# Kernel optimization log

Hardware: AMD Instinct MI355X
Metric: run time of the kernel (lower is better)

The kernel has to match this reference:

```python
import jax, jax.numpy as jnp
import numpy as np

B, N, IN_DIM, HID, OUT, E = 2, 50000, 64, 256, 128, 500000

def setup_inputs() -> dict:
    key = jax.random.key(0)
    ks = jax.random.split(key, 8)
    s = lambda fan_in: 1.0 / np.sqrt(fan_in)
    x = jax.random.normal(ks[0], (B, N, IN_DIM), dtype=jnp.float32)
    edges = jax.random.randint(ks[1], (E, 2), 0, N, dtype=jnp.int64)
    return {
        "x": x,
        "edges": edges,
        "ew1": jax.random.normal(ks[2], (2 * IN_DIM, HID), dtype=jnp.float32) * s(2 * IN_DIM),
        "eb1": jnp.zeros((HID,), jnp.float32),
        "ew2": jax.random.normal(ks[3], (HID, OUT), dtype=jnp.float32) * s(HID),
        "eb2": jnp.zeros((OUT,), jnp.float32),
        "nw1": jax.random.normal(ks[4], (IN_DIM, HID), dtype=jnp.float32) * s(IN_DIM),
        "nb1": jnp.zeros((HID,), jnp.float32),
        "nw2": jax.random.normal(ks[5], (HID, OUT), dtype=jnp.float32) * s(HID),
        "nb2": jnp.zeros((OUT,), jnp.float32),
        "dw": jax.random.normal(ks[6], (OUT, IN_DIM), dtype=jnp.float32) * s(OUT),
        "db": jnp.zeros((IN_DIM,), jnp.float32),
    }

def _mlp(z, w1, b1, w2, b2):
    return jax.nn.relu(z @ w1 + b1) @ w2 + b2

def reference(x, edges, ew1, eb1, ew2, eb2, nw1, nb1, nw2, nb2, dw, db):
    u, v = edges[:, 0], edges[:, 1]
    # node embedding: [B, N, OUT]
    h = _mlp(x, nw1, nb1, nw2, nb2)
    # per-edge MLP on concatenated endpoint features: [B, E, OUT]
    edge_input = jnp.concatenate([x[:, u], x[:, v]], axis=-1)  # [B, E, 2*IN]
    edge_emb = _mlp(edge_input, ew1, eb1, ew2, eb2)
    # scatter-add edge message to both endpoints
    messages = jnp.zeros_like(h).at[:, u].add(edge_emb).at[:, v].add(edge_emb)
    h = h + messages
    recon = h @ dw + db  # [B, N, IN]
    return recon
```

## Files before the change

### kernel.cpp

```cpp
#include <hip/hip_runtime.h>
#include <hip/hip_bf16.h>

#define BB   2
#define NN   50000
#define BN   100000
#define NE   500000
#define NSB  196

using u16 = unsigned short;
using u32 = unsigned int;
typedef __attribute__((ext_vector_type(8))) short short8;
typedef __attribute__((ext_vector_type(4))) float f32x4;

__device__ __forceinline__ u16 f2bf(float f) {
    union { float f; u32 u; } w; w.f = f;
    return (u16)((w.u + 0x7fffu + ((w.u >> 16) & 1u)) >> 16);
}

#if defined(__has_builtin)
#if __has_builtin(__builtin_amdgcn_cvt_pk_bf16_f32)
#define HAVE_CVTPK 1
#endif
#endif

__device__ __forceinline__ u32 pack_bf(float lo, float hi) {
#ifdef HAVE_CVTPK
    auto r = __builtin_amdgcn_cvt_pk_bf16_f32(lo, hi);
    u32 out; __builtin_memcpy(&out, &r, sizeof(out));
    return out;
#else
    return ((u32)f2bf(hi) << 16) | (u32)f2bf(lo);
#endif
}

__global__ __launch_bounds__(256) void csr_zero(int* __restrict__ cursor) {
    int i = blockIdx.x * 256 + threadIdx.x;
    if (i < NN) cursor[i] = 0;
}

__global__ __launch_bounds__(256) void csr_hist(const int* __restrict__ edges,
                                                int* __restrict__ cursor) {
    int e = blockIdx.x * 256 + threadIdx.x;
    if (e < NE) {
        atomicAdd(&cursor[edges[2*e]], 1);
        atomicAdd(&cursor[edges[2*e+1]], 1);
    }
}

__global__ __launch_bounds__(256) void scan_pass1(const int* __restrict__ cursor,
                                                  int* __restrict__ bsum) {
    __shared__ int s[256];
    const int t = threadIdx.x;
    int i = blockIdx.x * 256 + t;
    s[t] = (i < NN) ? cursor[i] : 0;
    __syncthreads();
    for (int d = 128; d > 0; d >>= 1) {
        if (t < d) s[t] += s[t + d];
        __syncthreads();
    }
    if (t == 0) bsum[blockIdx.x] = s[0];
}

__global__ __launch_bounds__(256) void scan_pass2(const int* __restrict__ bsum,
                                                  int* __restrict__ boff) {
    __shared__ int s[256];
    const int t = threadIdx.x;
    s[t] = (t < NSB) ? bsum[t] : 0;
    __syncthreads();
    for (int d = 1; d < 256; d <<= 1) {
        int v = (t >= d) ? s[t - d] : 0;
        __syncthreads();
        s[t] += v;
        __syncthreads();
    }
    if (t <= NSB) boff[t] = (t == 0) ? 0 : s[t - 1];
}

__global__ __launch_bounds__(256) void scan_pass3(int* __restrict__ cursor,
                                                  const int* __restrict__ boff,
                                                  int* __restrict__ off) {
    __shared__ int s[256];
    const int t = threadIdx.x;
    int i = blockIdx.x * 256 + t;
    int v = (i < NN) ? cursor[i] : 0;
    s[t] = v;
    __syncthreads();
    for (int d = 1; d < 256; d <<= 1) {
        int p = (t >= d) ? s[t - d] : 0;
        __syncthreads();
        s[t] += p;
        __syncthreads();
    }
    int excl = boff[blockIdx.x] + s[t] - v;
    if (i < NN) { off[i] = excl; cursor[i] = excl; }
    if (i == NN - 1) off[NN] = excl + v;
}

__global__ __launch_bounds__(256) void csr_fill(const int* __restrict__ edges,
                                                int* __restrict__ cursor,
                                                int* __restrict__ pos) {
    int e = blockIdx.x * 256 + threadIdx.x;
    if (e < NE) {
        pos[2*e]     = atomicAdd(&cursor[edges[2*e]], 1);
        pos[2*e + 1] = atomicAdd(&cursor[edges[2*e+1]], 1);
    }
}

__global__ __launch_bounds__(256) void weight_prep(
    const float* __restrict__ ew1, const float* __restrict__ nw1,
    const float* __restrict__ ew2, const float* __restrict__ nw2,
    const float* __restrict__ dw,  const float* __restrict__ db,
    const float* __restrict__ eb2, const float* __restrict__ nb2,
    u16* __restrict__ frag, float* __restrict__ bias2)
{
    int blk = blockIdx.x, t = threadIdx.x;
    if (blk < 192) {
        int idx = blk * 256 + t;
        const float* src; int KB, local;
        if (idx < 32768) { local = idx;         src = ew1; KB = 4; }
        else             { local = idx - 32768; src = nw1; KB = 2; }
        int j = local & 7, l = (local >> 3) & 63, rest = local >> 9;
        int kblk = rest % KB, ntile = rest / KB;
        int n = ntile * 16 + (l & 15);
        int k = kblk * 32 + ((l >> 4) << 3) + j;
        frag[idx] = f2bf(src[k * 256 + n]);
    } else if (blk < 320) {
        int idx = (blk - 192) * 256 + t;
        const float* src = (idx < 16384) ? ew2 : nw2;
        int local = idx & 16383;
        int j = local & 7, l = (local >> 3) & 63, rest = local >> 9;
        int kblk = rest & 7, ntile = rest >> 3;
        int n = ntile * 16 + (l & 15);
        int k = kblk * 32 + ((l >> 4) << 3) + j;
        float s = 0.f;
        for (int jj = 0; jj < 128; ++jj) s = fmaf(src[k * 128 + jj], dw[jj * 64 + n], s);
        frag[49152 + idx] = f2bf(s);
    } else if (t < 128) {
        int d = t & 63;
        const float* bsrc = (t >= 64) ? nb2 : eb2;
        float s = 0.f;
        #pragma unroll 4
        for (int j = 0; j < 128; ++j) s = fmaf(bsrc[j], dw[j * 64 + d], s);
        if (t >= 64) bias2[64 + d] = s + db[d];
        else         bias2[d] = s;
    }
}

__global__ __launch_bounds__(256) void node_mlp_kernel(
    const float* __restrict__ x, const float* __restrict__ nb1,
    const float* __restrict__ bias2, const u16* __restrict__ frag,
    u16* __restrict__ xbf, float* __restrict__ out)
{
    __shared__ u16 xs[64 * 64];
    __shared__ u16 hid[64 * 256];
    const int t = threadIdx.x;
    const int wave = t >> 6, l = t & 63, lane15 = l & 15, quad = l >> 4;
    const int r0 = blockIdx.x * 64;
    const int valid = min(64, BN - r0);

    #pragma unroll
    for (int it = 0; it < 4; ++it) {
        int i = t + it * 256;
        int m = i >> 4, c4 = i & 15;
        int row = min(r0 + m, BN - 1);
        float4 g = ((const float4*)x)[(size_t)row * 16 + c4];
        uint2 q = make_uint2(pack_bf(g.x, g.y), pack_bf(g.z, g.w));
        int chunk = c4 >> 1;
        *(uint2*)(xs + m * 64 + ((chunk ^ (m & 7)) << 3) + (c4 & 1) * 4) = q;
        *(uint2*)(xbf + (size_t)row * 64 + c4 * 4) = q;
    }
    __syncthreads();

    {
        f32x4 acc[4][4];
        #pragma unroll
        for (int i = 0; i < 4; ++i)
            #pragma unroll
            for (int mt = 0; mt < 4; ++mt) acc[i][mt] = f32x4{0.f,0.f,0.f,0.f};
        const u16* w1 = frag + 32768;
        #pragma unroll
        for (int kblk = 0; kblk < 2; ++kblk) {
            short8 bf[4], af[4];
            int chunk = kblk * 4 + quad;
            #pragma unroll
            for (int mt = 0; mt < 4; ++mt) {
                int row = mt*16 + lane15;
                bf[mt] = *(const short8*)(xs + row * 64 + ((chunk ^ (row & 7)) << 3));
            }
            #pragma unroll
            for (int i = 0; i < 4; ++i)
                af[i] = *(const short8*)(w1 + (((wave*4 + i)*2 + kblk)*64 + l) * 8);
            #pragma unroll
            for (int i = 0; i < 4; ++i)
                #pragma unroll
                for (int mt = 0; mt < 4; ++mt)
                    acc[i][mt] = __builtin_amdgcn_mfma_f32_16x16x32_bf16(af[i], bf[mt], acc[i][mt], 0, 0, 0);
        }
        #pragma unroll
        for (int i = 0; i < 4; ++i) {
            int n0 = (wave*4 + i)*16 + quad*4;
            int chunk = (wave*4 + i)*2 + (quad >> 1);
            float4 bv = *(const float4*)(nb1 + n0);
            #pragma unroll
            for (int mt = 0; mt < 4; ++mt) {
                int row = mt*16 + lane15;
                uint2 q = make_uint2(
                    pack_bf(fmaxf(acc[i][mt][0] + bv.x, 0.f), fmaxf(acc[i][mt][1] + bv.y, 0.f)),
                    pack_bf(fmaxf(acc[i][mt][2] + bv.z, 0.f), fmaxf(acc[i][mt][3] + bv.w, 0.f)));
                *(uint2*)(hid + row * 256 + ((chunk ^ (row & 15)) << 3) + (quad & 1) * 4) = q;
            }
        }
    }
    __syncthreads();

    {
        f32x4 acc[4];
        #pragma unroll
        for (int mt = 0; mt < 4; ++mt) acc[mt] = f32x4{0.f,0.f,0.f,0.f};
        const u16* w2 = frag + 65536;
        #pragma unroll
        for (int kblk = 0; kblk < 8; ++kblk) {
            short8 bf[4], af;
            int chunk = kblk * 4 + quad;
            #pragma unroll
            for (int mt = 0; mt < 4; ++mt) {
                int row = mt*16 + lane15;
                bf[mt] = *(const short8*)(hid + row * 256 + ((chunk ^ (row & 15)) << 3));
            }
            af = *(const short8*)(w2 + ((wave*8 + kblk)*64 + l) * 8);
            #pragma unroll
            for (int mt = 0; mt < 4; ++mt)
                acc[mt] = __builtin_amdgcn_mfma_f32_16x16x32_bf16(af, bf[mt], acc[mt], 0, 0, 0);
        }
        int n0 = wave*16 + quad*4;
        float4 bv = *(const float4*)(bias2 + 64 + n0);
        #pragma unroll
        for (int mt = 0; mt < 4; ++mt) {
            int m = mt*16 + lane15;
            if (m < valid) {
                float4 o;
                o.x = acc[mt][0] + bv.x; o.y = acc[mt][1] + bv.y;
                o.z = acc[mt][2] + bv.z; o.w = acc[mt][3] + bv.w;
                *(float4*)(out + (size_t)(r0 + m) * 64 + n0) = o;
            }
        }
    }
}

__global__ __launch_bounds__(256) void edge_emb_kernel(
    const u16* __restrict__ xbf, const int* __restrict__ edges,
    const float* __restrict__ eb1, const float* __restrict__ bias2,
    const u16* __restrict__ frag, const int* __restrict__ pos,
    u16* __restrict__ perm, int b_base, size_t pstride16)
{
    __shared__ u16 ein[64 * 128];
    __shared__ u16 hid[64 * 256];
    __shared__ int us[64], vs[64], ps[64], qs[64];
    const int t = threadIdx.x;
    const int wave = t >> 6, l = t & 63, lane15 = l & 15, quad = l >> 4;
    const int b = b_base + blockIdx.y;
    u16* permb = perm + pstride16 * blockIdx.y;
    const int e0 = blockIdx.x * 64;
    const int valid = min(64, NE - e0);

    if (t < 64) {
        int e = min(e0 + t, NE - 1);
        us[t] = edges[2 * e];
        vs[t] = edges[2 * e + 1];
        ps[t] = pos[2 * e];
        qs[t] = pos[2 * e + 1];
    }
    __syncthreads();

    #pragma unroll
    for (int it = 0; it < 4; ++it) {
        int i = t + it * 256;
        int m = i >> 4, c = i & 15;
        int half = c >> 3, c8 = c & 7;
        int node = half ? vs[m] : us[m];
        uint4 q = ((const uint4*)xbf)[(size_t)(b * NN + node) * 8 + c8];
        *(uint4*)(ein + m * 128 + ((c ^ (m & 15)) << 3)) = q;
    }
    __syncthreads();

    {
        f32x4 acc[4][4];
        #pragma unroll
        for (int i = 0; i < 4; ++i)
            #pragma unroll
            for (int mt = 0; mt < 4; ++mt) acc[i][mt] = f32x4{0.f,0.f,0.f,0.f};
        const u16* w1 = frag;
        #pragma unroll
        for (int kblk = 0; kblk < 4; ++kblk) {
            short8 bf[4], af[4];
            int chunk = kblk * 4 + quad;
            #pragma unroll
            for (int mt = 0; mt < 4; ++mt) {
                int row = mt*16 + lane15;
                bf[mt] = *(const short8*)(ein + row * 128 + ((chunk ^ (row & 15)) << 3));
            }
            #pragma unroll
            for (int i = 0; i < 4; ++i)
                af[i] = *(const short8*)(w1 + (((wave*4 + i)*4 + kblk)*64 + l) * 8);
            #pragma unroll
            for (int i = 0; i < 4; ++i)
                #pragma unroll
                for (int mt = 0; mt < 4; ++mt)
                    acc[i][mt] = __builtin_amdgcn_mfma_f32_16x16x32_bf16(af[i], bf[mt], acc[i][mt], 0, 0, 0);
        }
        #pragma unroll
        for (int i = 0; i < 4; ++i) {
            int n0 = (wave*4 + i)*16 + quad*4;
            int chunk = (wave*4 + i)*2 + (quad >> 1);
            float4 bv = *(const float4*)(eb1 + n0);
            #pragma unroll
            for (int mt = 0; mt < 4; ++mt) {
                int row = mt*16 + lane15;
                uint2 q = make_uint2(
                    pack_bf(fmaxf(acc[i][mt][0] + bv.x, 0.f), fmaxf(acc[i][mt][1] + bv.y, 0.f)),
                    pack_bf(fmaxf(acc[i][mt][2] + bv.z, 0.f), fmaxf(acc[i][mt][3] + bv.w, 0.f)));
                *(uint2*)(hid + row * 256 + ((chunk ^ (row & 15)) << 3) + (quad & 1) * 4) = q;
            }
        }
    }
    __syncthreads();

    {
        f32x4 acc[4];
        #pragma unroll
        for (int mt = 0; mt < 4; ++mt) acc[mt] = f32x4{0.f,0.f,0.f,0.f};
        const u16* w2 = frag + 49152;
        #pragma unroll
        for (int kblk = 0; kblk < 8; ++kblk) {
            short8 bf[4], af;
            int chunk = kblk * 4 + quad;
            #pragma unroll
            for (int mt = 0; mt < 4; ++mt) {
                int row = mt*16 + lane15;
                bf[mt] = *(const short8*)(hid + row * 256 + ((chunk ^ (row & 15)) << 3));
            }
            af = *(const short8*)(w2 + ((wave*8 + kblk)*64 + l) * 8);
            #pragma unroll
            for (int mt = 0; mt < 4; ++mt)
                acc[mt] = __builtin_amdgcn_mfma_f32_16x16x32_bf16(af, bf[mt], acc[mt], 0, 0, 0);
        }
        int n0 = wave*16 + quad*4;
        int chunk = wave*2 + (quad >> 1);
        float4 bv = *(const float4*)(bias2 + n0);
        #pragma unroll
        for (int mt = 0; mt < 4; ++mt) {
            int m = mt*16 + lane15;
            uint2 q = make_uint2(
                pack_bf(acc[mt][0] + bv.x, acc[mt][1] + bv.y),
                pack_bf(acc[mt][2] + bv.z, acc[mt][3] + bv.w));
            *(uint2*)(ein + m * 64 + ((chunk ^ (m & 7)) << 3) + (quad & 1) * 4) = q;
        }
    }
    __syncthreads();

    #pragma unroll
    for (int it = 0; it < 4; ++it) {
        int i = t + it * 256;
        int dest = i >> 3, c8 = i & 7;
        int m = dest >> 1;
        if (m < valid) {
            int p = (dest & 1) ? qs[m] : ps[m];
            ((uint4*)(permb + (size_t)p * 64))[c8] =
                *(const uint4*)(ein + m * 64 + ((c8 ^ (m & 7)) << 3));
        }
    }
}

__global__ __launch_bounds__(256) void gather_kernel(
    const u32* __restrict__ perm32, const int* __restrict__ off,
    float* __restrict__ out, int b_base, size_t pstride16)
{
    const int t = threadIdx.x, wave = t >> 6, l = t & 63;
    const int b = b_base + blockIdx.y;
    const u32* permb = perm32 + (pstride16 >> 1) * blockIdx.y;
    const int n = blockIdx.x * 4 + wave;
    const int base = off[n], cnt = off[n + 1] - base;
    if (cnt == 0) return;
    const int slot = l >> 4, c8h = l & 15;
    float a0 = 0.f, a1 = 0.f, a2 = 0.f, a3 = 0.f;
    for (int j0 = 0; j0 < cnt; j0 += 8) {
        int jA = j0 + slot, jB = j0 + 4 + slot;
        const u32* rpA = permb + (size_t)(base + min(jA, cnt - 1)) * 32 + 2 * c8h;
        const u32* rpB = permb + (size_t)(base + min(jB, cnt - 1)) * 32 + 2 * c8h;
        u32 wA0 = rpA[0], wA1 = rpA[1];
        u32 wB0 = rpB[0], wB1 = rpB[1];
        union { u32 u; float f; } x0, x1, x2, x3;
        if (jA < cnt) {
            x0.u = wA0 << 16; x1.u = wA0 & 0xffff0000u;
            x2.u = wA1 << 16; x3.u = wA1 & 0xffff0000u;
            a0 += x0.f; a1 += x1.f; a2 += x2.f; a3 += x3.f;
        }
        if (jB < cnt) {
            x0.u = wB0 << 16; x1.u = wB0 & 0xffff0000u;
            x2.u = wB1 << 16; x3.u = wB1 & 0xffff0000u;
            a0 += x0.f; a1 += x1.f; a2 += x2.f; a3 += x3.f;
        }
    }
    a0 += __shfl_xor(a0, 16); a1 += __shfl_xor(a1, 16);
    a2 += __shfl_xor(a2, 16); a3 += __shfl_xor(a3, 16);
    a0 += __shfl_xor(a0, 32); a1 += __shfl_xor(a1, 32);
    a2 += __shfl_xor(a2, 32); a3 += __shfl_xor(a3, 32);
    if (l < 16) {
        float4* p = (float4*)(out + (size_t)(b * NN + n) * 64 + 4 * l);
        float4 h = *p;
        h.x += a0; h.y += a1; h.z += a2; h.w += a3;
        *p = h;
    }
}

extern "C" void kernel_launch(void* const* d_in, const int* in_sizes, int n_in,
                              void* d_out, int out_size, void* d_ws, size_t ws_size,
                              hipStream_t stream) {
    const float* x     = (const float*)d_in[0];
    const int*   edges = (const int*)d_in[1];
    const float* ew1   = (const float*)d_in[2];
    const float* eb1   = (const float*)d_in[3];
    const float* ew2   = (const float*)d_in[4];
    const float* eb2   = (const float*)d_in[5];
    const float* nw1   = (const float*)d_in[6];
    const float* nb1   = (const float*)d_in[7];
    const float* nw2   = (const float*)d_in[8];
    const float* nb2   = (const float*)d_in[9];
    const float* dw    = (const float*)d_in[10];
    const float* db    = (const float*)d_in[11];
    float* out = (float*)d_out;

    char* w = (char*)d_ws;
    size_t o = 0;
    auto take = [&](size_t bytes) { char* p = w + o; o = (o + bytes + 511) & ~(size_t)511; return p; };
    u16*   frag   = (u16*)  take(81920 * 2);
    float* bias2  = (float*)take(128 * 4);
    int*   cursor = (int*)  take((size_t)NN * 4);
    int*   off    = (int*)  take((size_t)(NN + 1) * 4);
    int*   bsum   = (int*)  take((size_t)(NSB + 1) * 4);
    int*   boff   = (int*)  take((size_t)(NSB + 1) * 4);
    int*   pos    = (int*)  take((size_t)2 * NE * 4);
    u16*   xbf    = (u16*)  take((size_t)BN * 64 * 2);
    const size_t permElems = (size_t)2 * NE * 64;
    u16*   perm   = (u16*)  take(permElems * 2);
    bool dual = (o + permElems * 2) <= ws_size;
    if (dual) take(permElems * 2);

    csr_zero<<<NSB, 256, 0, stream>>>(cursor);
    csr_hist<<<(NE + 255) / 256, 256, 0, stream>>>(edges, cursor);
    scan_pass1<<<NSB, 256, 0, stream>>>(cursor, bsum);
    scan_pass2<<<1, 256, 0, stream>>>(bsum, boff);
    scan_pass3<<<NSB, 256, 0, stream>>>(cursor, boff, off);
    csr_fill<<<(NE + 255) / 256, 256, 0, stream>>>(edges, cursor, pos);

    weight_prep<<<321, 256, 0, stream>>>(ew1, nw1, ew2, nw2, dw, db, eb2, nb2, frag, bias2);

    node_mlp_kernel<<<(BN + 63) / 64, 256, 0, stream>>>(x, nb1, bias2, frag, xbf, out);

    if (dual) {
        edge_emb_kernel<<<dim3((NE + 63) / 64, BB), 256, 0, stream>>>(
            xbf, edges, eb1, bias2, frag, pos, perm, 0, permElems);
        gather_kernel<<<dim3(NN / 4, BB), 256, 0, stream>>>(
            (const u32*)perm, off, out, 0, permElems);
    } else {
        for (int b = 0; b < BB; ++b) {
            edge_emb_kernel<<<dim3((NE + 63) / 64, 1), 256, 0, stream>>>(
                xbf, edges, eb1, bias2, frag, pos, perm, b, 0);
            gather_kernel<<<dim3(NN / 4, 1), 256, 0, stream>>>(
                (const u32*)perm, off, out, b, 0);
        }
    }
}
```

Before: 444.8 us.

## Precompute per-node first-layer edge projections and gather them per edge

The first edge-MLP layer splits into top and bottom halves of ew1 applied to x[u] and x[v]. These halves are computed once per node into fp16 tables At/Ab, and each edge then only gathers, adds and applies relu before the second GEMM, which now runs in fp16. The CSR now stores edge indices instead of scatter positions, so edge embeddings are written contiguously and the gather reads them through eidx. The gains are fewer first-layer FLOPs and no scattered writes. The costs are per-node table traffic of 256 fp16 values per row, processing the batches sequentially, and fp16 range/precision risk in the hidden layer.

```diff
diff --git a/kernel.cpp b/kernel.cpp
--- a/kernel.cpp
+++ b/kernel.cpp
@@ -10,16 +10,23 @@
 using u16 = unsigned short;
 using u32 = unsigned int;
 typedef __attribute__((ext_vector_type(8))) short short8;
+typedef __attribute__((ext_vector_type(8))) _Float16 half8;
 typedef __attribute__((ext_vector_type(4))) float f32x4;
 
 __device__ __forceinline__ u16 f2bf(float f) {
     union { float f; u32 u; } w; w.f = f;
     return (u16)((w.u + 0x7fffu + ((w.u >> 16) & 1u)) >> 16);
 }
+__device__ __forceinline__ u16 f2h(float f) {
+    _Float16 h = (_Float16)f; u16 u; __builtin_memcpy(&u, &h, 2); return u;
+}
 
 #if defined(__has_builtin)
 #if __has_builtin(__builtin_amdgcn_cvt_pk_bf16_f32)
 #define HAVE_CVTPK 1
+#endif
+#if __has_builtin(__builtin_amdgcn_cvt_pkrtz)
+#define HAVE_PKRTZ 1
 #endif
 #endif
 
@@ -33,6 +40,27 @@
 #endif
 }
 
+__device__ __forceinline__ u32 pack_h2(float lo, float hi) {
+#ifdef HAVE_PKRTZ
+    auto r = __builtin_amdgcn_cvt_pkrtz(lo, hi);
+    u32 out; __builtin_memcpy(&out, &r, sizeof(out));
+    return out;
+#else
+    return ((u32)f2h(hi) << 16) | (u32)f2h(lo);
+#endif
+}
+
+__device__ __forceinline__ u32 pk_add_h2(u32 a, u32 b) {
+    u32 d; asm("v_pk_add_f16 %0, %1, %2" : "=v"(d) : "v"(a), "v"(b)); return d;
+}
+__device__ __forceinline__ u32 pk_relu_h2(u32 a) {
+    u32 d, z = 0u;
+    asm("v_pk_max_f16 %0, %1, %2" : "=v"(d) : "v"(a), "v"(z)); return d;
+}
+__device__ __forceinline__ half8 as_h8(short8 s) {
+    half8 h; __builtin_memcpy(&h, &s, 16); return h;
+}
+
 __global__ __launch_bounds__(256) void csr_zero(int* __restrict__ cursor) {
     int i = blockIdx.x * 256 + threadIdx.x;
     if (i < NN) cursor[i] = 0;
@@ -98,11 +126,13 @@
 
 __global__ __launch_bounds__(256) void csr_fill(const int* __restrict__ edges,
                                                 int* __restrict__ cursor,
-                                                int* __restrict__ pos) {
+                                                int* __restrict__ eidx) {
     int e = blockIdx.x * 256 + threadIdx.x;
     if (e < NE) {
-        pos[2*e]     = atomicAdd(&cursor[edges[2*e]], 1);
-        pos[2*e + 1] = atomicAdd(&cursor[edges[2*e+1]], 1);
+        int s0 = atomicAdd(&cursor[edges[2*e]], 1);
+        eidx[s0] = e;
+        int s1 = atomicAdd(&cursor[edges[2*e+1]], 1);
+        eidx[s1] = e;
     }
 }
 
@@ -126,7 +156,8 @@
         frag[idx] = f2bf(src[k * 256 + n]);
     } else if (blk < 320) {
         int idx = (blk - 192) * 256 + t;
-        const float* src = (idx < 16384) ? ew2 : nw2;
+        bool is_e = (idx < 16384);
+        const float* src = is_e ? ew2 : nw2;
         int local = idx & 16383;
         int j = local & 7, l = (local >> 3) & 63, rest = local >> 9;
         int kblk = rest & 7, ntile = rest >> 3;
@@ -134,7 +165,7 @@
         int k = kblk * 32 + ((l >> 4) << 3) + j;
         float s = 0.f;
         for (int jj = 0; jj < 128; ++jj) s = fmaf(src[k * 128 + jj], dw[jj * 64 + n], s);
-        frag[49152 + idx] = f2bf(s);
+        frag[49152 + idx] = is_e ? f2h(s) : f2bf(s);
     } else if (t < 128) {
         int d = t & 63;
         const float* bsrc = (t >= 64) ? nb2 : eb2;
@@ -247,19 +278,93 @@
     }
 }
 
-__global__ __launch_bounds__(256) void edge_emb_kernel(
-    const u16* __restrict__ xbf, const int* __restrict__ edges,
-    const float* __restrict__ eb1, const float* __restrict__ bias2,
-    const u16* __restrict__ frag, const int* __restrict__ pos,
-    u16* __restrict__ perm, int b_base, size_t pstride16)
+__global__ __launch_bounds__(256) void edge_pre_kernel(
+    const u16* __restrict__ xbf, const float* __restrict__ eb1,
+    const u16* __restrict__ frag, u16* __restrict__ At, u16* __restrict__ Ab,
+    int b)
 {
-    __shared__ u16 ein[64 * 128];
-    __shared__ u16 hid[64 * 256];
-    __shared__ int us[64], vs[64], ps[64], qs[64];
+    __shared__ u16 xs[64 * 64];
+    __shared__ u16 stg[64 * 256];
     const int t = threadIdx.x;
     const int wave = t >> 6, l = t & 63, lane15 = l & 15, quad = l >> 4;
-    const int b = b_base + blockIdx.y;
-    u16* permb = perm + pstride16 * blockIdx.y;
+    const int r0 = blockIdx.x * 64;
+    const int valid = min(64, NN - r0);
+
+    #pragma unroll
+    for (int it = 0; it < 2; ++it) {
+        int i = t + it * 256;
+        int m = i >> 3, c = i & 7;
+        int row = min(r0 + m, NN - 1);
+        uint4 q = ((const uint4*)xbf)[((size_t)(b * NN + row)) * 8 + c];
+        *(uint4*)(xs + m * 64 + ((c ^ (m & 7)) << 3)) = q;
+    }
+    __syncthreads();
+
+    const u16* w1 = frag;
+    for (int T = 0; T < 2; ++T) {
+        f32x4 acc[4][4];
+        #pragma unroll
+        for (int i = 0; i < 4; ++i)
+            #pragma unroll
+            for (int mt = 0; mt < 4; ++mt) acc[i][mt] = f32x4{0.f,0.f,0.f,0.f};
+        #pragma unroll
+        for (int kblk = 0; kblk < 2; ++kblk) {
+            short8 bf[4], af[4];
+            int chunk = kblk * 4 + quad;
+            #pragma unroll
+            for (int mt = 0; mt < 4; ++mt) {
+                int row = mt*16 + lane15;
+                bf[mt] = *(const short8*)(xs + row * 64 + ((chunk ^ (row & 7)) << 3));
+            }
+            #pragma unroll
+            for (int i = 0; i < 4; ++i)
+                af[i] = *(const short8*)(w1 + (((wave*4 + i)*4 + T*2 + kblk)*64 + l) * 8);
+            #pragma unroll
+            for (int i = 0; i < 4; ++i)
+                #pragma unroll
+                for (int mt = 0; mt < 4; ++mt)
+                    acc[i][mt] = __builtin_amdgcn_mfma_f32_16x16x32_bf16(af[i], bf[mt], acc[i][mt], 0, 0, 0);
+        }
+        #pragma unroll
+        for (int i = 0; i < 4; ++i) {
+            int ntile = wave*4 + i;
+            int n0 = ntile*16 + quad*4;
+            float4 bv;
+            if (T == 0) bv = *(const float4*)(eb1 + n0);
+            else        bv = make_float4(0.f, 0.f, 0.f, 0.f);
+            int c16 = ntile*2 + (quad >> 1);
+            #pragma unroll
+            for (int mt = 0; mt < 4; ++mt) {
+                int row = mt*16 + lane15;
+                uint2 q = make_uint2(
+                    pack_h2(acc[i][mt][0] + bv.x, acc[i][mt][1] + bv.y),
+                    pack_h2(acc[i][mt][2] + bv.z, acc[i][mt][3] + bv.w));
+                *(uint2*)(stg + row * 256 + ((c16 ^ (row & 7)) << 3) + (quad & 1) * 4) = q;
+            }
+        }
+        __syncthreads();
+        u16* dst = (T == 0) ? At : Ab;
+        #pragma unroll
+        for (int it = 0; it < 8; ++it) {
+            int i = t + it * 256;
+            int m = i >> 5, c = i & 31;
+            if (m < valid)
+                ((uint4*)dst)[((size_t)(r0 + m)) * 32 + c] =
+                    *(const uint4*)(stg + m * 256 + ((c ^ (m & 7)) << 3));
+        }
+        __syncthreads();
+    }
+}
+
+__global__ __launch_bounds__(256) void edge_emb2_kernel(
+    const u16* __restrict__ At, const u16* __restrict__ Ab,
+    const int* __restrict__ edges, const float* __restrict__ bias2,
+    const u16* __restrict__ frag, u16* __restrict__ perm)
+{
+    __shared__ u16 hid[64 * 256];
+    __shared__ int us[64], vs[64];
+    const int t = threadIdx.x;
+    const int wave = t >> 6, l = t & 63, lane15 = l & 15, quad = l >> 4;
     const int e0 = blockIdx.x * 64;
     const int valid = min(64, NE - e0);
 
@@ -267,83 +372,46 @@
         int e = min(e0 + t, NE - 1);
         us[t] = edges[2 * e];
         vs[t] = edges[2 * e + 1];
-        ps[t] = pos[2 * e];
-        qs[t] = pos[2 * e + 1];
     }
     __syncthreads();
 
     #pragma unroll
-    for (int it = 0; it < 4; ++it) {
+    for (int it = 0; it < 8; ++it) {
         int i = t + it * 256;
-        int m = i >> 4, c = i & 15;
-        int half = c >> 3, c8 = c & 7;
-        int node = half ? vs[m] : us[m];
-        uint4 q = ((const uint4*)xbf)[(size_t)(b * NN + node) * 8 + c8];
-        *(uint4*)(ein + m * 128 + ((c ^ (m & 15)) << 3)) = q;
+        int m = i >> 5, c = i & 31;
+        int u = us[m], v = vs[m];
+        uint4 a = ((const uint4*)At)[(size_t)((u32)u * 32 + c)];
+        uint4 bq = ((const uint4*)Ab)[(size_t)((u32)v * 32 + c)];
+        uint4 r;
+        r.x = pk_relu_h2(pk_add_h2(a.x, bq.x));
+        r.y = pk_relu_h2(pk_add_h2(a.y, bq.y));
+        r.z = pk_relu_h2(pk_add_h2(a.z, bq.z));
+        r.w = pk_relu_h2(pk_add_h2(a.w, bq.w));
+        *(uint4*)(hid + m * 256 + ((c ^ (m & 15)) << 3)) = r;
+    }
+    __syncthreads();
+
+    f32x4 acc[4];
+    #pragma unroll
+    for (int mt = 0; mt < 4; ++mt) acc[mt] = f32x4{0.f,0.f,0.f,0.f};
+    const u16* w2 = frag + 49152;
+    #pragma unroll
+    for (int kblk = 0; kblk < 8; ++kblk) {
+        short8 bf[4], af;
+        int chunk = kblk * 4 + quad;
+        #pragma unroll
+        for (int mt = 0; mt < 4; ++mt) {
+            int row = mt*16 + lane15;
+            bf[mt] = *(const short8*)(hid + row * 256 + ((chunk ^ (row & 15)) << 3));
+        }
+        af = *(const short8*)(w2 + ((wave*8 + kblk)*64 + l) * 8);
+        #pragma unroll
+        for (int mt = 0; mt < 4; ++mt)
+            acc[mt] = __builtin_amdgcn_mfma_f32_16x16x32_f16(as_h8(af), as_h8(bf[mt]), acc[mt], 0, 0, 0);
     }
     __syncthreads();
 
     {
-        f32x4 acc[4][4];
-        #pragma unroll
-        for (int i = 0; i < 4; ++i)
-            #pragma unroll
-            for (int mt = 0; mt < 4; ++mt) acc[i][mt] = f32x4{0.f,0.f,0.f,0.f};
-        const u16* w1 = frag;
-        #pragma unroll
-        for (int kblk = 0; kblk < 4; ++kblk) {
-            short8 bf[4], af[4];
-            int chunk = kblk * 4 + quad;
-            #pragma unroll
-            for (int mt = 0; mt < 4; ++mt) {
-                int row = mt*16 + lane15;
-                bf[mt] = *(const short8*)(ein + row * 128 + ((chunk ^ (row & 15)) << 3));
-            }
-            #pragma unroll
-            for (int i = 0; i < 4; ++i)
-                af[i] = *(const short8*)(w1 + (((wave*4 + i)*4 + kblk)*64 + l) * 8);
-            #pragma unroll
-            for (int i = 0; i < 4; ++i)
-                #pragma unroll
-                for (int mt = 0; mt < 4; ++mt)
-                    acc[i][mt] = __builtin_amdgcn_mfma_f32_16x16x32_bf16(af[i], bf[mt], acc[i][mt], 0, 0, 0);
-        }
-        #pragma unroll
-        for (int i = 0; i < 4; ++i) {
-            int n0 = (wave*4 + i)*16 + quad*4;
-            int chunk = (wave*4 + i)*2 + (quad >> 1);
-            float4 bv = *(const float4*)(eb1 + n0);
-            #pragma unroll
-            for (int mt = 0; mt < 4; ++mt) {
-                int row = mt*16 + lane15;
-                uint2 q = make_uint2(
-                    pack_bf(fmaxf(acc[i][mt][0] + bv.x, 0.f), fmaxf(acc[i][mt][1] + bv.y, 0.f)),
-                    pack_bf(fmaxf(acc[i][mt][2] + bv.z, 0.f), fmaxf(acc[i][mt][3] + bv.w, 0.f)));
-                *(uint2*)(hid + row * 256 + ((chunk ^ (row & 15)) << 3) + (quad & 1) * 4) = q;
-            }
-        }
-    }
-    __syncthreads();
-
-    {
-        f32x4 acc[4];
-        #pragma unroll
-        for (int mt = 0; mt < 4; ++mt) acc[mt] = f32x4{0.f,0.f,0.f,0.f};
-        const u16* w2 = frag + 49152;
-        #pragma unroll
-        for (int kblk = 0; kblk < 8; ++kblk) {
-            short8 bf[4], af;
-            int chunk = kblk * 4 + quad;
-            #pragma unroll
-            for (int mt = 0; mt < 4; ++mt) {
-                int row = mt*16 + lane15;
-                bf[mt] = *(const short8*)(hid + row * 256 + ((chunk ^ (row & 15)) << 3));
-            }
-            af = *(const short8*)(w2 + ((wave*8 + kblk)*64 + l) * 8);
-            #pragma unroll
-            for (int mt = 0; mt < 4; ++mt)
-                acc[mt] = __builtin_amdgcn_mfma_f32_16x16x32_bf16(af, bf[mt], acc[mt], 0, 0, 0);
-        }
         int n0 = wave*16 + quad*4;
         int chunk = wave*2 + (quad >> 1);
         float4 bv = *(const float4*)(bias2 + n0);
@@ -353,31 +421,26 @@
             uint2 q = make_uint2(
                 pack_bf(acc[mt][0] + bv.x, acc[mt][1] + bv.y),
                 pack_bf(acc[mt][2] + bv.z, acc[mt][3] + bv.w));
-            *(uint2*)(ein + m * 64 + ((chunk ^ (m & 7)) << 3) + (quad & 1) * 4) = q;
+            *(uint2*)(hid + m * 64 + ((chunk ^ (m & 7)) << 3) + (quad & 1) * 4) = q;
         }
     }
     __syncthreads();
 
     #pragma unroll
-    for (int it = 0; it < 4; ++it) {
+    for (int it = 0; it < 2; ++it) {
         int i = t + it * 256;
-        int dest = i >> 3, c8 = i & 7;
-        int m = dest >> 1;
-        if (m < valid) {
-            int p = (dest & 1) ? qs[m] : ps[m];
-            ((uint4*)(permb + (size_t)p * 64))[c8] =
-                *(const uint4*)(ein + m * 64 + ((c8 ^ (m & 7)) << 3));
-        }
-    }
-}
-
-__global__ __launch_bounds__(256) void gather_kernel(
+        int m = i >> 3, c8 = i & 7;
+        if (m < valid)
+            ((uint4*)perm)[((size_t)(e0 + m)) * 8 + c8] =
+                *(const uint4*)(hid + m * 64 + ((c8 ^ (m & 7)) << 3));
+    }
+}
+
+__global__ __launch_bounds__(256) void gather2_kernel(
     const u32* __restrict__ perm32, const int* __restrict__ off,
-    float* __restrict__ out, int b_base, size_t pstride16)
+    const int* __restrict__ eidx, float* __restrict__ out, int b)
 {
     const int t = threadIdx.x, wave = t >> 6, l = t & 63;
-    const int b = b_base + blockIdx.y;
-    const u32* permb = perm32 + (pstride16 >> 1) * blockIdx.y;
     const int n = blockIdx.x * 4 + wave;
     const int base = off[n], cnt = off[n + 1] - base;
     if (cnt == 0) return;
@@ -385,8 +448,10 @@
     float a0 = 0.f, a1 = 0.f, a2 = 0.f, a3 = 0.f;
     for (int j0 = 0; j0 < cnt; j0 += 8) {
         int jA = j0 + slot, jB = j0 + 4 + slot;
-        const u32* rpA = permb + (size_t)(base + min(jA, cnt - 1)) * 32 + 2 * c8h;
-        const u32* rpB = permb + (size_t)(base + min(jB, cnt - 1)) * 32 + 2 * c8h;
+        int eA = eidx[base + min(jA, cnt - 1)];
+        int eB = eidx[base + min(jB, cnt - 1)];
+        const u32* rpA = perm32 + (size_t)eA * 32 + 2 * c8h;
+        const u32* rpB = perm32 + (size_t)eB * 32 + 2 * c8h;
         u32 wA0 = rpA[0], wA1 = rpA[1];
         u32 wB0 = rpB[0], wB1 = rpB[1];
         union { u32 u; float f; } x0, x1, x2, x3;
@@ -439,35 +504,26 @@
     int*   off    = (int*)  take((size_t)(NN + 1) * 4);
     int*   bsum   = (int*)  take((size_t)(NSB + 1) * 4);
     int*   boff   = (int*)  take((size_t)(NSB + 1) * 4);
-    int*   pos    = (int*)  take((size_t)2 * NE * 4);
+    int*   eidx   = (int*)  take((size_t)2 * NE * 4);
     u16*   xbf    = (u16*)  take((size_t)BN * 64 * 2);
-    const size_t permElems = (size_t)2 * NE * 64;
-    u16*   perm   = (u16*)  take(permElems * 2);
-    bool dual = (o + permElems * 2) <= ws_size;
-    if (dual) take(permElems * 2);
+    u16*   At     = (u16*)  take((size_t)NN * 256 * 2);
+    u16*   Ab     = (u16*)  take((size_t)NN * 256 * 2);
+    u16*   perm   = (u16*)  take((size_t)NE * 64 * 2);
 
     csr_zero<<<NSB, 256, 0, stream>>>(cursor);
     csr_hist<<<(NE + 255) / 256, 256, 0, stream>>>(edges, cursor);
     scan_pass1<<<NSB, 256, 0, stream>>>(cursor, bsum);
     scan_pass2<<<1, 256, 0, stream>>>(bsum, boff);
     scan_pass3<<<NSB, 256, 0, stream>>>(cursor, boff, off);
-    csr_fill<<<(NE + 255) / 256, 256, 0, stream>>>(edges, cursor, pos);
+    csr_fill<<<(NE + 255) / 256, 256, 0, stream>>>(edges, cursor, eidx);
 
     weight_prep<<<321, 256, 0, stream>>>(ew1, nw1, ew2, nw2, dw, db, eb2, nb2, frag, bias2);
 
     node_mlp_kernel<<<(BN + 63) / 64, 256, 0, stream>>>(x, nb1, bias2, frag, xbf, out);
 
-    if (dual) {
-        edge_emb_kernel<<<dim3((NE + 63) / 64, BB), 256, 0, stream>>>(
-            xbf, edges, eb1, bias2, frag, pos, perm, 0, permElems);
-        gather_kernel<<<dim3(NN / 4, BB), 256, 0, stream>>>(
-            (const u32*)perm, off, out, 0, permElems);
-    } else {
-        for (int b = 0; b < BB; ++b) {
-            edge_emb_kernel<<<dim3((NE + 63) / 64, 1), 256, 0, stream>>>(
-                xbf, edges, eb1, bias2, frag, pos, perm, b, 0);
-            gather_kernel<<<dim3(NN / 4, 1), 256, 0, stream>>>(
-                (const u32*)perm, off, out, b, 0);
-        }
-    }
-}
+    for (int b = 0; b < BB; ++b) {
+        edge_pre_kernel<<<(NN + 63) / 64, 256, 0, stream>>>(xbf, eb1, frag, At, Ab, b);
+        edge_emb2_kernel<<<(NE + 63) / 64, 256, 0, stream>>>(At, Ab, edges, bias2, frag, perm);
+        gather2_kernel<<<NN / 4, 256, 0, stream>>>((const u32*)perm, off, eidx, out, b);
+    }
+}
```

New measurement: 508.6 us. 1.14x slower.
